# Kernel optimization log

Measured on AMD Instinct MI355X. Metric: run time of the kernel, lower is better.

## Reference

```python
import jax, jax.numpy as jnp
import numpy as np

V = 32000      # vocab
TMAX = 1024    # BLOCK_SIZE
D = 768        # N_EMBD
H = 12         # N_HEAD
L = 12         # N_LAYER
HS = D // H    # head_size
FF = 4 * D
B, T = 4, 1024


def setup_inputs() -> dict:
    key = jax.random.key(0)
    ks = iter(jax.random.split(key, 40))
    n = lambda shape: 0.02 * jax.random.normal(next(ks), shape, dtype=jnp.float32)
    return dict(
        idx=jax.random.randint(next(ks), (B, T), 0, V),
        targets=jax.random.randint(next(ks), (B, T), 0, V),
        tok_emb=n((V, D)),
        pos_emb=n((TMAX, D)),
        Wq=n((L, H, D, HS)), Wk=n((L, H, D, HS)), Wv=n((L, H, D, HS)),
        Wo=n((L, D, D)), bo=jnp.zeros((L, D)),
        W1=n((L, D, FF)), b1=jnp.zeros((L, FF)),
        W2=n((L, FF, D)), b2=jnp.zeros((L, D)),
        ln1_g=jnp.ones((L, D)), ln1_b=jnp.zeros((L, D)),
        ln2_g=jnp.ones((L, D)), ln2_b=jnp.zeros((L, D)),
        lnf_g=jnp.ones((D,)), lnf_b=jnp.zeros((D,)),
        Wlm=n((D, V)), blm=jnp.zeros((V,)),
    )


def _ln(x, g, b, eps=1e-5):
    m = x.mean(-1, keepdims=True)
    v = x.var(-1, keepdims=True)
    return (x - m) * jax.lax.rsqrt(v + eps) * g + b


def reference(idx, targets, tok_emb, pos_emb, Wq, Wk, Wv, Wo, bo,
              W1, b1, W2, b2, ln1_g, ln1_b, ln2_g, ln2_b, lnf_g, lnf_b,
              Wlm, blm):
    Bsz, Tt = idx.shape
    x = tok_emb[idx] + pos_emb[:Tt]                      # [B,T,D]
    causal = jnp.tril(jnp.ones((Tt, Tt), dtype=bool))     # [T,T]

    def layer(x, p):
        wq, wk, wv, wo, bob, w1, b1b, w2, b2b, g1, be1, g2, be2 = p
        h = _ln(x, g1, be1)
        q = jnp.einsum('btd,hdk->bhtk', h, wq)
        k = jnp.einsum('btd,hdk->bhtk', h, wk)
        v = jnp.einsum('btd,hdk->bhtk', h, wv)
        wei = jnp.einsum('bhtk,bhsk->bhts', q, k) * (HS ** -0.5)
        wei = jnp.where(causal, wei, -jnp.inf)
        wei = jax.nn.softmax(wei, axis=-1)                # dropout=0 in eval
        att = jnp.einsum('bhts,bhsk->bhtk', wei, v)
        att = att.transpose(0, 2, 1, 3).reshape(Bsz, Tt, H * HS)  # concat heads
        x = x + att @ wo + bob
        h2 = _ln(x, g2, be2)
        x = x + jax.nn.relu(h2 @ w1 + b1b) @ w2 + b2b
        return x, None

    x, _ = jax.lax.scan(layer, x,
                        (Wq, Wk, Wv, Wo, bo, W1, b1, W2, b2,
                         ln1_g, ln1_b, ln2_g, ln2_b))
    x = _ln(x, lnf_g, lnf_b)
    logits = x @ Wlm + blm                                # [B,T,V]
    lf = logits.reshape(Bsz * Tt, V)
    tf = targets.reshape(-1)
    logp = jax.nn.log_softmax(lf, axis=-1)
    loss = -jnp.take_along_axis(logp, tf[:, None], axis=1).mean()
    return lf, loss
```

## Files before the change

### kernel.cpp

```cpp
#include <hip/hip_runtime.h>

constexpr int C_B   = 4;
constexpr int C_T   = 1024;
constexpr int C_D   = 768;
constexpr int C_H   = 12;
constexpr int C_HS  = 64;
constexpr int C_FF  = 3072;
constexpr int C_V   = 32000;
constexpr int C_L   = 12;
constexpr int ROWS  = C_B * C_T;
constexpr int QKVN  = 3 * C_D;
constexpr int NCB   = C_V / 256;

typedef __bf16 bf16;
typedef __attribute__((ext_vector_type(8))) __bf16 bf16x8;
typedef __attribute__((ext_vector_type(4))) float  f32x4;
typedef __attribute__((ext_vector_type(4))) short  s16x4;

static __device__ __forceinline__ void gload16(const void* g, void* l) {
  __builtin_amdgcn_global_load_lds((const __attribute__((address_space(1))) void*)g,
                                   (__attribute__((address_space(3))) void*)l,
                                   16, 0, 0);
}

__global__ __launch_bounds__(256) void embed_kernel(const int* __restrict__ idx,
    const float* __restrict__ tok, const float* __restrict__ pos, float* __restrict__ x) {
  int gid = blockIdx.x * 256 + threadIdx.x;
  int row = gid / C_D, d = gid - row * C_D;
  int t = row & (C_T - 1);
  x[gid] = tok[(long)idx[row] * C_D + d] + pos[(long)t * C_D + d];
}

__global__ __launch_bounds__(256) void ln_kernel(const float* __restrict__ x,
    const float* __restrict__ g, const float* __restrict__ bb, long goff,
    bf16* __restrict__ out) {
  int row = blockIdx.x, tid = threadIdx.x;
  const float* xr = x + (long)row * C_D;
  float v0 = xr[tid], v1 = xr[tid + 256], v2 = xr[tid + 512];
  float s = v0 + v1 + v2;
  float s2 = v0 * v0 + v1 * v1 + v2 * v2;
#pragma unroll
  for (int off = 32; off > 0; off >>= 1) {
    s  += __shfl_down(s, off);
    s2 += __shfl_down(s2, off);
  }
  __shared__ float sm[4], sq[4];
  if ((tid & 63) == 0) { sm[tid >> 6] = s; sq[tid >> 6] = s2; }
  __syncthreads();
  s  = sm[0] + sm[1] + sm[2] + sm[3];
  s2 = sq[0] + sq[1] + sq[2] + sq[3];
  float mean = s * (1.f / C_D);
  float var  = s2 * (1.f / C_D) - mean * mean;
  float rstd = rsqrtf(var + 1e-5f);
  bf16* orow = out + (long)row * C_D;
  orow[tid]       = (bf16)((v0 - mean) * rstd * g[goff + tid]       + bb[goff + tid]);
  orow[tid + 256] = (bf16)((v1 - mean) * rstd * g[goff + tid + 256] + bb[goff + tid + 256]);
  orow[tid + 512] = (bf16)((v2 - mean) * rstd * g[goff + tid + 512] + bb[goff + tid + 512]);
}

__global__ __launch_bounds__(256) void transpose_kernel(const float* __restrict__ src,
    bf16* __restrict__ dst, int K, int N, long soff0, int ntn) {
  __shared__ bf16 tile[32][33];
  const float* s = src + soff0;
  int tn = blockIdx.x % ntn, tk = blockIdx.x / ntn;
  int c = threadIdx.x & 31, r = threadIdx.x >> 5;
#pragma unroll
  for (int it = 0; it < 4; ++it)
    tile[r + 8 * it][c] = (bf16)s[(long)(tk * 32 + r + 8 * it) * N + tn * 32 + c];
  __syncthreads();
#pragma unroll
  for (int it = 0; it < 4; ++it)
    dst[(long)(tn * 32 + r + 8 * it) * K + tk * 32 + c] = tile[c][r + 8 * it];
}

__global__ __launch_bounds__(256) void transpose_layer_kernel(
    const float* __restrict__ Wq, const float* __restrict__ Wk,
    const float* __restrict__ Wv, const float* __restrict__ Wo,
    const float* __restrict__ W1, const float* __restrict__ W2,
    bf16* __restrict__ wqkvt, bf16* __restrict__ wot,
    bf16* __restrict__ w1t, bf16* __restrict__ w2t, int l) {
  int bid = blockIdx.x;
  const float* src; bf16* dst; int K, N, ntn, t;
  if (bid < 1728) {
    int which = bid / 576, r = bid % 576, head = r / 48;
    t = r % 48;
    const float* W = which == 0 ? Wq : which == 1 ? Wk : Wv;
    src = W + (long)l * C_H * C_D * C_HS + (long)head * C_D * C_HS;
    dst = wqkvt + (long)which * C_D * C_D + (long)head * C_HS * C_D;
    K = C_D; N = C_HS; ntn = 2;
  } else if (bid < 2304) {
    t = bid - 1728; src = Wo + (long)l * C_D * C_D; dst = wot;
    K = C_D; N = C_D; ntn = 24;
  } else if (bid < 4608) {
    t = bid - 2304; src = W1 + (long)l * C_D * C_FF; dst = w1t;
    K = C_D; N = C_FF; ntn = 96;
  } else {
    t = bid - 4608; src = W2 + (long)l * C_FF * C_D; dst = w2t;
    K = C_FF; N = C_D; ntn = 24;
  }
  __shared__ bf16 tile[32][33];
  int tn = t % ntn, tk = t / ntn;
  int c = threadIdx.x & 31, r = threadIdx.x >> 5;
#pragma unroll
  for (int it = 0; it < 4; ++it)
    tile[r + 8 * it][c] = (bf16)src[(long)(tk * 32 + r + 8 * it) * N + tn * 32 + c];
  __syncthreads();
#pragma unroll
  for (int it = 0; it < 4; ++it)
    dst[(long)(tn * 32 + r + 8 * it) * K + tk * 32 + c] = tile[c][r + 8 * it];
}

__global__ __launch_bounds__(512) void gemm256(const bf16* __restrict__ A,
    const bf16* __restrict__ Bt, const float* __restrict__ bias, long boff,
    float* __restrict__ outp, float* __restrict__ lossp, int N, int K) {
  __shared__ __attribute__((aligned(16))) char smem[131072];
  int tid = threadIdx.x;
  int l = tid & 63, w = tid >> 6;
  int wm = w >> 2, wn = w & 3;
  int lg = l >> 4, lr = l & 15;

  int nwg = gridDim.x;
  int fid = blockIdx.x;
  int swz = (fid & 7) * (nwg >> 3) + (fid >> 3);
  long row0 = (long)(swz & 15) * 256;
  long col0 = (long)(swz >> 4) * 256;
  int cbi = (int)(col0 >> 8);

  int Y0 = tid * 16, Y1 = 8192 + tid * 16;
  auto dec = [](int Y, int& R, int& C) {
    int s = Y >> 10, y = Y & 1023;
    int r15 = y >> 6, z = y & 63;
    int q = (z ^ ((r15 & 8) << 2)) >> 4;
    R = (s >> 1) * 16 + r15;
    C = (s & 1) * 32 + q * 8;
  };
  int R0, C0, R1, C1;
  dec(Y0, R0, C0);  dec(Y1, R1, C1);
  const bf16* Ab = A  + row0 * K;
  const bf16* Bb = Bt + col0 * K;

  auto stage = [&](int d, int kt) {
    char* bb = smem + d * 65536;
    long kc = (long)kt * 64;
    gload16(Ab + (long)R0 * K + kc + C0, bb + Y0);
    gload16(Ab + (long)R1 * K + kc + C1, bb + Y1);
    gload16(Ab + (long)(128 + R0) * K + kc + C0, bb + 16384 + Y0);
    gload16(Ab + (long)(128 + R1) * K + kc + C1, bb + 16384 + Y1);
    gload16(Bb + (long)R0 * K + kc + C0, bb + 32768 + Y0);
    gload16(Bb + (long)R1 * K + kc + C1, bb + 32768 + Y1);
    gload16(Bb + (long)(128 + R0) * K + kc + C0, bb + 49152 + Y0);
    gload16(Bb + (long)(128 + R1) * K + kc + C1, bb + 49152 + Y1);
  };

  f32x4 acc[8][4];
  const f32x4 fz = {0.f, 0.f, 0.f, 0.f};
#pragma unroll
  for (int mf = 0; mf < 8; ++mf)
#pragma unroll
    for (int nf = 0; nf < 4; ++nf) acc[mf][nf] = fz;

  int aoff = lr * 64 + ((lg * 16) ^ ((lr & 8) << 2));
  int nk = K >> 6;
  stage(0, 0);
  int d = 0;
  for (int kt = 0; kt < nk; ++kt) {
    __syncthreads();
    if (kt + 1 < nk) stage(d ^ 1, kt + 1);
    const char* bB = smem + d * 65536 + 32768 + (wn >> 1) * 16384;
    bf16x8 bfrag[4][2];
#pragma unroll
    for (int nf = 0; nf < 4; ++nf)
#pragma unroll
      for (int k = 0; k < 2; ++k)
        bfrag[nf][k] = *(const bf16x8*)(bB + ((((wn & 1) * 4 + nf) * 2 + k) << 10) + aoff);
#pragma unroll
    for (int p = 0; p < 4; ++p) {
      bf16x8 af[2][2];
#pragma unroll
      for (int mi = 0; mi < 2; ++mi)
#pragma unroll
        for (int k = 0; k < 2; ++k) {
          int f = p * 2 + mi;
          const char* aB = smem + d * 65536 + (f >> 2) * 16384;
          af[mi][k] = *(const bf16x8*)(aB + (((wm * 4 + (f & 3)) * 2 + k) << 10) + aoff);
        }
      __builtin_amdgcn_s_setprio(1);
#pragma unroll
      for (int mi = 0; mi < 2; ++mi)
#pragma unroll
        for (int nf = 0; nf < 4; ++nf)
#pragma unroll
          for (int k = 0; k < 2; ++k)
            acc[p * 2 + mi][nf] = __builtin_amdgcn_mfma_f32_16x16x32_bf16(
                af[mi][k], bfrag[nf][k], acc[p * 2 + mi][nf], 0, 0, 0);
      __builtin_amdgcn_s_setprio(0);
    }
    d ^= 1;
  }
  __syncthreads();

#pragma unroll
  for (int h = 0; h < 2; ++h) {
    if (h) __syncthreads();
    float* lf = (float*)smem;
#pragma unroll
    for (int fq = 0; fq < 4; ++fq) {
      int f = h * 4 + fq;
      int rl = wm * 64 + fq * 16 + lg * 4;
#pragma unroll
      for (int nf = 0; nf < 4; ++nf) {
        int col = wn * 64 + nf * 16 + lr;
        float bv = bias ? bias[boff + col0 + col] : 0.f;
#pragma unroll
        for (int r = 0; r < 4; ++r)
          lf[(rl + r) * 256 + col] = acc[f][nf][r] + bv;
      }
    }
    __syncthreads();
#pragma unroll
    for (int it = 0; it < 16; ++it) {
      int byte = it * 8192 + tid * 16;
      int rl = byte >> 10, cb = byte & 1023;
      *(f32x4*)(outp + (row0 + h * 128 + rl) * N + col0 + (cb >> 2)) =
          *(const f32x4*)(smem + byte);
    }
    if (lossp) {
      const float* lfc = (const float*)smem;
      int row = tid >> 2, chunk = tid & 3;
      float M = -1e30f, S = 0.f;
#pragma unroll
      for (int j = 0; j < 16; ++j) {
        int jj = (j + row) & 15;
        f32x4 v = *(const f32x4*)(lfc + row * 256 + chunk * 64 + jj * 4);
#pragma unroll
        for (int q = 0; q < 4; ++q) {
          float xv = v[q];
          if (xv > M) { S *= __expf(M - xv); M = xv; }
          S += __expf(xv - M);
        }
      }
#pragma unroll
      for (int off = 1; off < 4; off <<= 1) {
        float Mo = __shfl_xor(M, off), So = __shfl_xor(S, off);
        float Mn = fmaxf(M, Mo);
        S = S * __expf(M - Mn) + So * __expf(Mo - Mn);
        M = Mn;
      }
      if (chunk == 0) {
        long pi = ((row0 + h * 128 + row) * NCB + cbi) * 2;
        lossp[pi] = M;  lossp[pi + 1] = S;
      }
    }
  }
}

template <int MODE>
__global__ __launch_bounds__(256) void gemm_bt(const bf16* __restrict__ A,
    const bf16* __restrict__ Bt, const float* __restrict__ bias, long boff,
    void* __restrict__ outp, float* __restrict__ resid, int N, int K) {
  __shared__ __attribute__((aligned(16))) char smem[32768];
  int tid = threadIdx.x;
  int l = tid & 63;
  int w = tid >> 6, wr = w >> 1, wc = w & 1;
  int lg = l >> 4, lr = l & 15;

  int nwg = gridDim.x;
  int fid = blockIdx.x;
  int swz = (fid & 7) * (nwg >> 3) + (fid >> 3);
  long row0 = (long)(swz & 31) * 128;
  long col0 = (long)(swz >> 5) * 128;

  const bf16* ga = A  + (row0 + (tid >> 2)) * K + (tid & 3) * 8;
  const bf16* gb = Bt + (col0 + (tid >> 2)) * K + (tid & 3) * 8;

  f32x4 acc[4][4];
  const f32x4 fz = {0.f, 0.f, 0.f, 0.f};
#pragma unroll
  for (int m = 0; m < 4; ++m)
#pragma unroll
    for (int n = 0; n < 4; ++n) acc[m][n] = fz;

  int nk = K >> 5;
  {
    bf16* la = (bf16*)smem + tid * 8;
    bf16* lb = (bf16*)(smem + 8192) + tid * 8;
    gload16(ga, la);  gload16(ga + (long)64 * K, la + 2048);
    gload16(gb, lb);  gload16(gb + (long)64 * K, lb + 2048);
    ga += 32; gb += 32;
  }
  int cur = 0;
  for (int t = 0; t < nk; ++t) {
    __syncthreads();
    if (t + 1 < nk) {
      char* bufb = smem + (cur ^ 1) * 16384;
      bf16* la = (bf16*)bufb + tid * 8;
      bf16* lb = (bf16*)(bufb + 8192) + tid * 8;
      gload16(ga, la);  gload16(ga + (long)64 * K, la + 2048);
      gload16(gb, lb);  gload16(gb + (long)64 * K, lb + 2048);
      ga += 32; gb += 32;
    }
    const bf16* cA = (const bf16*)(smem + cur * 16384);
    const bf16* cB = (const bf16*)(smem + cur * 16384 + 8192);
    bf16x8 af[4], bfr[4];
#pragma unroll
    for (int m = 0; m < 4; ++m)
      af[m] = *(const bf16x8*)(cA + (wr * 64 + m * 16 + lr) * 32 + lg * 8);
#pragma unroll
    for (int n = 0; n < 4; ++n)
      bfr[n] = *(const bf16x8*)(cB + (wc * 64 + n * 16 + lr) * 32 + lg * 8);
#pragma unroll
    for (int m = 0; m < 4; ++m)
#pragma unroll
      for (int n = 0; n < 4; ++n)
        acc[m][n] = __builtin_amdgcn_mfma_f32_16x16x32_bf16(af[m], bfr[n], acc[m][n], 0, 0, 0);
    cur ^= 1;
  }
  __syncthreads();

  if (MODE == 0 || MODE == 1) {
    bf16* lc = (bf16*)smem;
#pragma unroll
    for (int n = 0; n < 4; ++n) {
      int gcl = wc * 64 + n * 16 + lr;
      float bv = bias ? bias[boff + col0 + gcl] : 0.f;
#pragma unroll
      for (int m = 0; m < 4; ++m) {
        int rb = wr * 64 + m * 16 + lg * 4;
#pragma unroll
        for (int r = 0; r < 4; ++r) {
          float v = acc[m][n][r] + bv;
          if (MODE == 1) v = fmaxf(v, 0.f);
          lc[(rb + r) * 128 + gcl] = (bf16)v;
        }
      }
    }
    __syncthreads();
#pragma unroll
    for (int it = 0; it < 8; ++it) {
      int byte = it * 4096 + tid * 16;
      int rl = byte >> 8;
      int cb = byte & 255;
      *(bf16x8*)((bf16*)outp + (row0 + rl) * N + col0 + (cb >> 1)) =
          *(const bf16x8*)(smem + byte);
    }
  } else {
#pragma unroll
    for (int pair = 0; pair < 2; ++pair) {
      float* lcf = (float*)smem;
#pragma unroll
      for (int n = 0; n < 4; ++n) {
        int gcl = wc * 64 + n * 16 + lr;
        float bv = bias ? bias[boff + col0 + gcl] : 0.f;
#pragma unroll
        for (int mi = 0; mi < 2; ++mi) {
          int m = pair * 2 + mi;
          int rl = wr * 32 + mi * 16 + lg * 4;
#pragma unroll
          for (int r = 0; r < 4; ++r)
            lcf[(rl + r) * 128 + gcl] = acc[m][n][r] + bv;
        }
      }
      __syncthreads();
#pragma unroll
      for (int it = 0; it < 8; ++it) {
        int byte = it * 4096 + tid * 16;
        int rl = byte >> 9;
        int cb = byte & 511;
        long gr = row0 + (rl >> 5) * 64 + pair * 32 + ((rl >> 4) & 1) * 16 + (rl & 15);
        f32x4 v = *(const f32x4*)(smem + byte);
        f32x4 g = *(const f32x4*)(resid + gr * N + col0 + (cb >> 2));
        v += g;
        *(f32x4*)(resid + gr * N + col0 + (cb >> 2)) = v;
      }
      __syncthreads();
    }
  }
}

#define TRRD(D, OFF) asm volatile("ds_read_b64_tr_b16 %0, %1 offset:" OFF \
                                  : "=v"(D) : "v"(trp))
__global__ __launch_bounds__(64) void attn_kernel(const bf16* __restrict__ qkv,
                                                  bf16* __restrict__ attout) {
  int fid = blockIdx.x;
  int swzb = (fid & 7) * 384 + (fid >> 3);
  int qt = swzb & 63;
  int bh = swzb >> 6;
  int b = bh / C_H, h = bh % C_H;
  int l = threadIdx.x;
  int lg = l >> 4, lr = l & 15;
  const bf16* base = qkv + (long)b * C_T * QKVN;

  const bf16* qp = base + (long)(qt * 16 + lr) * QKVN + h * C_HS;
  bf16x8 qf0 = *(const bf16x8*)(qp + lg * 8);
  bf16x8 qf1 = *(const bf16x8*)(qp + 32 + lg * 8);

  const f32x4 fz = {0.f, 0.f, 0.f, 0.f};
  f32x4 o[4] = {fz, fz, fz, fz};
  float m_run[4], l_run[4];
#pragma unroll
  for (int r = 0; r < 4; ++r) { m_run[r] = -1e30f; l_run[r] = 0.f; }

  __shared__ __attribute__((aligned(16))) bf16 p_lds[16][40];
  __shared__ __attribute__((aligned(16))) bf16 vt_sub[2048];

  unsigned trp = (unsigned)(unsigned long)
      ((const __attribute__((address_space(3))) char*)vt_sub + l * 8);

  int nkt = (qt * 16 + 15) / 32 + 1;
  for (int kt = 0; kt < nkt; ++kt) {
    int key0 = kt * 32;
    f32x4 sacc[2];
#pragma unroll
    for (int ss = 0; ss < 2; ++ss) {
      const bf16* kp = base + (long)(key0 + ss * 16 + lr) * QKVN + C_D + h * C_HS;
      bf16x8 kf0 = *(const bf16x8*)(kp + lg * 8);
      bf16x8 kf1 = *(const bf16x8*)(kp + 32 + lg * 8);
      f32x4 a = fz;
      a = __builtin_amdgcn_mfma_f32_16x16x32_bf16(qf0, kf0, a, 0, 0, 0);
      a = __builtin_amdgcn_mfma_f32_16x16x32_bf16(qf1, kf1, a, 0, 0, 0);
      sacc[ss] = a;
    }
#pragma unroll
    for (int r = 0; r < 4; ++r) {
      int qrow = qt * 16 + lg * 4 + r;
      bool u0 = (key0 + lr) <= qrow;
      bool u1 = (key0 + 16 + lr) <= qrow;
      float s0 = u0 ? sacc[0][r] * 0.125f : -1e30f;
      float s1 = u1 ? sacc[1][r] * 0.125f : -1e30f;
      float mr = fmaxf(s0, s1);
      mr = fmaxf(mr, __shfl_xor(mr, 1));
      mr = fmaxf(mr, __shfl_xor(mr, 2));
      mr = fmaxf(mr, __shfl_xor(mr, 4));
      mr = fmaxf(mr, __shfl_xor(mr, 8));
      float mnew = fmaxf(m_run[r], mr);
      float scale = __expf(m_run[r] - mnew);
      float p0 = u0 ? __expf(s0 - mnew) : 0.f;
      float p1 = u1 ? __expf(s1 - mnew) : 0.f;
      float rs = p0 + p1;
      rs += __shfl_xor(rs, 1);
      rs += __shfl_xor(rs, 2);
      rs += __shfl_xor(rs, 4);
      rs += __shfl_xor(rs, 8);
      l_run[r] = l_run[r] * scale + rs;
      m_run[r] = mnew;
      o[0][r] *= scale; o[1][r] *= scale; o[2][r] *= scale; o[3][r] *= scale;
      p_lds[lg * 4 + r][lr]      = (bf16)p0;
      p_lds[lg * 4 + r][16 + lr] = (bf16)p1;
    }
#pragma unroll
    for (int it = 0; it < 4; ++it) {
      int kl = it * 8 + (l >> 3);
      int d0 = (l & 7) * 8;
      bf16x8 vv = *(const bf16x8*)(base + (long)(key0 + kl) * QKVN + 2 * C_D + h * C_HS + d0);
      int ba = ((d0 >> 4) << 10) + (((kl >> 2) & 1) << 9) + ((kl >> 3) << 7)
             + ((kl & 3) << 5) + ((d0 & 15) << 1);
      *(bf16x8*)((char*)vt_sub + ba) = vv;
    }
    __syncthreads();
    s16x4 t0a, t0b, t1a, t1b, t2a, t2b, t3a, t3b;
    TRRD(t0a, "0");    TRRD(t0b, "512");
    TRRD(t1a, "1024"); TRRD(t1b, "1536");
    TRRD(t2a, "2048"); TRRD(t2b, "2560");
    TRRD(t3a, "3072"); TRRD(t3b, "3584");
    bf16x8 pf = *(const bf16x8*)(&p_lds[lr][lg * 8]);
    asm volatile("s_waitcnt lgkmcnt(0)" ::: "memory");
    __builtin_amdgcn_sched_barrier(0);
    union uu { short s[8]; bf16x8 v; };
    auto mk = [](s16x4 a, s16x4 bq) {
      uu u;
      u.s[0] = a[0]; u.s[1] = a[1]; u.s[2] = a[2]; u.s[3] = a[3];
      u.s[4] = bq[0]; u.s[5] = bq[1]; u.s[6] = bq[2]; u.s[7] = bq[3];
      return u.v;
    };
    o[0] = __builtin_amdgcn_mfma_f32_16x16x32_bf16(pf, mk(t0a, t0b), o[0], 0, 0, 0);
    o[1] = __builtin_amdgcn_mfma_f32_16x16x32_bf16(pf, mk(t1a, t1b), o[1], 0, 0, 0);
    o[2] = __builtin_amdgcn_mfma_f32_16x16x32_bf16(pf, mk(t2a, t2b), o[2], 0, 0, 0);
    o[3] = __builtin_amdgcn_mfma_f32_16x16x32_bf16(pf, mk(t3a, t3b), o[3], 0, 0, 0);
    __syncthreads();
  }
#pragma unroll
  for (int c = 0; c < 4; ++c)
#pragma unroll
    for (int r = 0; r < 4; ++r) {
      int qrow = qt * 16 + lg * 4 + r;
      attout[((long)b * C_T + qrow) * C_D + h * C_HS + c * 16 + lr] =
          (bf16)(o[c][r] / l_run[r]);
    }
}

__global__ __launch_bounds__(128) void loss_partial_kernel(const float* __restrict__ lossp,
    const float* __restrict__ logits, const int* __restrict__ targets,
    float* __restrict__ rowloss) {
  int row = blockIdx.x * 128 + threadIdx.x;
  const float* pp = lossp + (long)row * NCB * 2;
  float M = -1e30f, S = 0.f;
  for (int i = 0; i < NCB; ++i) {
    float pm = pp[i * 2], ps = pp[i * 2 + 1];
    float Mn = fmaxf(M, pm);
    S = S * __expf(M - Mn) + ps * __expf(pm - Mn);
    M = Mn;
  }
  float lt = logits[(long)row * C_V + targets[row]];
  rowloss[row] = -(lt - M - logf(S));
}

__global__ __launch_bounds__(256) void loss_final(const float* __restrict__ rowloss,
                                                  float* __restrict__ out) {
  int tid = threadIdx.x;
  float s = 0.f;
  for (int i = tid; i < ROWS; i += 256) s += rowloss[i];
#pragma unroll
  for (int off = 32; off > 0; off >>= 1) s += __shfl_down(s, off);
  __shared__ float sm[4];
  if ((tid & 63) == 0) sm[tid >> 6] = s;
  __syncthreads();
  if (tid == 0) out[0] = (sm[0] + sm[1] + sm[2] + sm[3]) * (1.f / ROWS);
}

extern "C" void kernel_launch(void* const* d_in, const int* in_sizes, int n_in,
                              void* d_out, int out_size, void* d_ws, size_t ws_size,
                              hipStream_t stream) {
  (void)in_sizes; (void)n_in; (void)out_size; (void)ws_size;
  const int*   idx     = (const int*)  d_in[0];
  const int*   targets = (const int*)  d_in[1];
  const float* tok     = (const float*)d_in[2];
  const float* pos     = (const float*)d_in[3];
  const float* Wq      = (const float*)d_in[4];
  const float* Wk      = (const float*)d_in[5];
  const float* Wv      = (const float*)d_in[6];
  const float* Wo      = (const float*)d_in[7];
  const float* bo      = (const float*)d_in[8];
  const float* W1      = (const float*)d_in[9];
  const float* b1      = (const float*)d_in[10];
  const float* W2      = (const float*)d_in[11];
  const float* b2      = (const float*)d_in[12];
  const float* ln1g    = (const float*)d_in[13];
  const float* ln1b    = (const float*)d_in[14];
  const float* ln2g    = (const float*)d_in[15];
  const float* ln2b    = (const float*)d_in[16];
  const float* lnfg    = (const float*)d_in[17];
  const float* lnfb    = (const float*)d_in[18];
  const float* Wlm     = (const float*)d_in[19];
  const float* blm     = (const float*)d_in[20];

  char* p = (char*)d_ws;
  auto alloc = [&](size_t bytes) {
    char* r = p; p += (bytes + 255) & ~(size_t)255; return r;
  };
  float* x       = (float*)alloc((size_t)ROWS * C_D * 4);
  bf16*  h       = (bf16*) alloc((size_t)ROWS * C_D * 2);
  bf16*  qkv     = (bf16*) alloc((size_t)ROWS * QKVN * 2);
  bf16*  attout  = (bf16*) alloc((size_t)ROWS * C_D * 2);
  bf16*  ffbuf   = (bf16*) alloc((size_t)ROWS * C_FF * 2);
  bf16*  wqkvt   = (bf16*) alloc((size_t)QKVN * C_D * 2);
  bf16*  wot     = (bf16*) alloc((size_t)C_D * C_D * 2);
  bf16*  w1t     = (bf16*) alloc((size_t)C_FF * C_D * 2);
  bf16*  w2t     = (bf16*) alloc((size_t)C_D * C_FF * 2);
  float* rowloss = (float*)alloc((size_t)ROWS * 4);
  float* lossp   = (float*)alloc((size_t)ROWS * NCB * 2 * 4);
  bf16*  wlmt    = qkv;

  float* logits = (float*)d_out;

  embed_kernel<<<ROWS * C_D / 256, 256, 0, stream>>>(idx, tok, pos, x);

  for (int l = 0; l < C_L; ++l) {
    transpose_layer_kernel<<<6912, 256, 0, stream>>>(
        Wq, Wk, Wv, Wo, W1, W2, wqkvt, wot, w1t, w2t, l);

    ln_kernel<<<ROWS, 256, 0, stream>>>(x, ln1g, ln1b, (long)l * C_D, h);
    gemm_bt<0><<<(QKVN / 128) * 32, 256, 0, stream>>>(
        h, wqkvt, nullptr, 0, qkv, nullptr, QKVN, C_D);
    attn_kernel<<<C_B * C_H * (C_T / 16), 64, 0, stream>>>(qkv, attout);
    gemm_bt<2><<<(C_D / 128) * 32, 256, 0, stream>>>(
        attout, wot, bo, (long)l * C_D, nullptr, x, C_D, C_D);
    ln_kernel<<<ROWS, 256, 0, stream>>>(x, ln2g, ln2b, (long)l * C_D, h);
    gemm_bt<1><<<(C_FF / 128) * 32, 256, 0, stream>>>(
        h, w1t, b1, (long)l * C_FF, ffbuf, nullptr, C_FF, C_D);
    gemm_bt<2><<<(C_D / 128) * 32, 256, 0, stream>>>(
        ffbuf, w2t, b2, (long)l * C_D, nullptr, x, C_D, C_FF);
  }

  transpose_kernel<<<(C_V / 32) * (C_D / 32), 256, 0, stream>>>(
      Wlm, wlmt, C_D, C_V, 0, C_V / 32);

  ln_kernel<<<ROWS, 256, 0, stream>>>(x, lnfg, lnfb, 0, h);
  gemm256<<<16 * (C_V / 256), 512, 0, stream>>>(
      h, wlmt, blm, 0, logits, lossp, C_V, C_D);
  loss_partial_kernel<<<ROWS / 128, 128, 0, stream>>>(lossp, logits, targets, rowloss);
  loss_final<<<1, 256, 0, stream>>>(rowloss, logits + (long)ROWS * C_V);
}
```

Before: 2.981 ms.

## Add 128x64 residual GEMM kernel and split-barrier LM-head pipeline

Adds a new gemm_bt64 kernel with 128x64 tiles for the two N=768 residual-add GEMMs (attention output and FFN down projection), doubling the workgroup count from 192 to 384 so more CUs are used. Its epilogue writes the full fp32 tile in one pass instead of two. The LM-head GEMM loop now issues the next stage's loads, waits with an explicit vmcnt, and uses a raw s_barrier pair in place of __syncthreads, so the wait on outstanding global-to-LDS loads is controlled by hand. The smaller tiles lower reuse per workgroup, and the hand-written waitcnt depends on exactly how many loads stage issues.

```diff
diff --git a/kernel.cpp b/kernel.cpp
--- a/kernel.cpp
+++ b/kernel.cpp
@@ -164,8 +164,17 @@
   stage(0, 0);
   int d = 0;
   for (int kt = 0; kt < nk; ++kt) {
-    __syncthreads();
-    if (kt + 1 < nk) stage(d ^ 1, kt + 1);
+    __builtin_amdgcn_s_barrier();
+    asm volatile("" ::: "memory");
+    if (kt + 1 < nk) {
+      stage(d ^ 1, kt + 1);
+      asm volatile("s_waitcnt vmcnt(8)" ::: "memory");
+    } else {
+      asm volatile("s_waitcnt vmcnt(0)" ::: "memory");
+    }
+    __builtin_amdgcn_s_barrier();
+    asm volatile("" ::: "memory");
+
     const char* bB = smem + d * 65536 + 32768 + (wn >> 1) * 16384;
     bf16x8 bfrag[4][2];
 #pragma unroll
@@ -257,7 +266,7 @@
 template <int MODE>
 __global__ __launch_bounds__(256) void gemm_bt(const bf16* __restrict__ A,
     const bf16* __restrict__ Bt, const float* __restrict__ bias, long boff,
-    void* __restrict__ outp, float* __restrict__ resid, int N, int K) {
+    void* __restrict__ outp, int N, int K) {
   __shared__ __attribute__((aligned(16))) char smem[32768];
   int tid = threadIdx.x;
   int l = tid & 63;
@@ -317,63 +326,119 @@
   }
   __syncthreads();
 
-  if (MODE == 0 || MODE == 1) {
-    bf16* lc = (bf16*)smem;
-#pragma unroll
-    for (int n = 0; n < 4; ++n) {
-      int gcl = wc * 64 + n * 16 + lr;
-      float bv = bias ? bias[boff + col0 + gcl] : 0.f;
-#pragma unroll
-      for (int m = 0; m < 4; ++m) {
-        int rb = wr * 64 + m * 16 + lg * 4;
-#pragma unroll
-        for (int r = 0; r < 4; ++r) {
-          float v = acc[m][n][r] + bv;
-          if (MODE == 1) v = fmaxf(v, 0.f);
-          lc[(rb + r) * 128 + gcl] = (bf16)v;
-        }
+  bf16* lc = (bf16*)smem;
+#pragma unroll
+  for (int n = 0; n < 4; ++n) {
+    int gcl = wc * 64 + n * 16 + lr;
+    float bv = bias ? bias[boff + col0 + gcl] : 0.f;
+#pragma unroll
+    for (int m = 0; m < 4; ++m) {
+      int rb = wr * 64 + m * 16 + lg * 4;
+#pragma unroll
+      for (int r = 0; r < 4; ++r) {
+        float v = acc[m][n][r] + bv;
+        if (MODE == 1) v = fmaxf(v, 0.f);
+        lc[(rb + r) * 128 + gcl] = (bf16)v;
       }
     }
+  }
+  __syncthreads();
+#pragma unroll
+  for (int it = 0; it < 8; ++it) {
+    int byte = it * 4096 + tid * 16;
+    int rl = byte >> 8;
+    int cb = byte & 255;
+    *(bf16x8*)((bf16*)outp + (row0 + rl) * N + col0 + (cb >> 1)) =
+        *(const bf16x8*)(smem + byte);
+  }
+}
+
+__global__ __launch_bounds__(256) void gemm_bt64(const bf16* __restrict__ A,
+    const bf16* __restrict__ Bt, const float* __restrict__ bias, long boff,
+    float* __restrict__ resid, int N, int K) {
+  __shared__ __attribute__((aligned(16))) char smem[32768];
+  int tid = threadIdx.x;
+  int l = tid & 63;
+  int w = tid >> 6, wr = w >> 1, wc = w & 1;
+  int lg = l >> 4, lr = l & 15;
+
+  int nwg = gridDim.x;
+  int fid = blockIdx.x;
+  int swz = (fid & 7) * (nwg >> 3) + (fid >> 3);
+  long row0 = (long)(swz & 31) * 128;
+  long col0 = (long)(swz >> 5) * 64;
+
+  const bf16* ga = A  + (row0 + (tid >> 2)) * K + (tid & 3) * 8;
+  const bf16* gb = Bt + (col0 + (tid >> 2)) * K + (tid & 3) * 8;
+
+  f32x4 acc[4][2];
+  const f32x4 fz = {0.f, 0.f, 0.f, 0.f};
+#pragma unroll
+  for (int m = 0; m < 4; ++m)
+#pragma unroll
+    for (int n = 0; n < 2; ++n) acc[m][n] = fz;
+
+  int nk = K >> 5;
+  {
+    bf16* la = (bf16*)smem + tid * 8;
+    bf16* lb = (bf16*)(smem + 8192) + tid * 8;
+    gload16(ga, la);  gload16(ga + (long)64 * K, la + 2048);
+    if (tid < 256) gload16(gb, lb);
+    ga += 32; gb += 32;
+  }
+  int cur = 0;
+  for (int t = 0; t < nk; ++t) {
     __syncthreads();
-#pragma unroll
-    for (int it = 0; it < 8; ++it) {
-      int byte = it * 4096 + tid * 16;
-      int rl = byte >> 8;
-      int cb = byte & 255;
-      *(bf16x8*)((bf16*)outp + (row0 + rl) * N + col0 + (cb >> 1)) =
-          *(const bf16x8*)(smem + byte);
-    }
-  } else {
-#pragma unroll
-    for (int pair = 0; pair < 2; ++pair) {
-      float* lcf = (float*)smem;
-#pragma unroll
-      for (int n = 0; n < 4; ++n) {
-        int gcl = wc * 64 + n * 16 + lr;
-        float bv = bias ? bias[boff + col0 + gcl] : 0.f;
-#pragma unroll
-        for (int mi = 0; mi < 2; ++mi) {
-          int m = pair * 2 + mi;
-          int rl = wr * 32 + mi * 16 + lg * 4;
-#pragma unroll
-          for (int r = 0; r < 4; ++r)
-            lcf[(rl + r) * 128 + gcl] = acc[m][n][r] + bv;
-        }
-      }
-      __syncthreads();
-#pragma unroll
-      for (int it = 0; it < 8; ++it) {
-        int byte = it * 4096 + tid * 16;
-        int rl = byte >> 9;
-        int cb = byte & 511;
-        long gr = row0 + (rl >> 5) * 64 + pair * 32 + ((rl >> 4) & 1) * 16 + (rl & 15);
-        f32x4 v = *(const f32x4*)(smem + byte);
-        f32x4 g = *(const f32x4*)(resid + gr * N + col0 + (cb >> 2));
-        v += g;
-        *(f32x4*)(resid + gr * N + col0 + (cb >> 2)) = v;
-      }
-      __syncthreads();
-    }
+    if (t + 1 < nk) {
+      char* bufb = smem + (cur ^ 1) * 12288;
+      bf16* la = (bf16*)bufb + tid * 8;
+      bf16* lb = (bf16*)(bufb + 8192) + tid * 8;
+      gload16(ga, la);  gload16(ga + (long)64 * K, la + 2048);
+      gload16(gb, lb);
+      ga += 32; gb += 32;
+    }
+    const bf16* cA = (const bf16*)(smem + cur * 12288);
+    const bf16* cB = (const bf16*)(smem + cur * 12288 + 8192);
+    bf16x8 af[4], bfr[2];
+#pragma unroll
+    for (int m = 0; m < 4; ++m)
+      af[m] = *(const bf16x8*)(cA + (wr * 64 + m * 16 + lr) * 32 + lg * 8);
+#pragma unroll
+    for (int n = 0; n < 2; ++n)
+      bfr[n] = *(const bf16x8*)(cB + (wc * 32 + n * 16 + lr) * 32 + lg * 8);
+#pragma unroll
+    for (int m = 0; m < 4; ++m)
+#pragma unroll
+      for (int n = 0; n < 2; ++n)
+        acc[m][n] = __builtin_amdgcn_mfma_f32_16x16x32_bf16(af[m], bfr[n], acc[m][n], 0, 0, 0);
+    cur ^= 1;
+  }
+  __syncthreads();
+
+  float* lcf = (float*)smem;
+#pragma unroll
+  for (int n = 0; n < 2; ++n) {
+    int col = wc * 32 + n * 16 + lr;
+    float bv = bias ? bias[boff + col0 + col] : 0.f;
+#pragma unroll
+    for (int m = 0; m < 4; ++m) {
+      int rl = wr * 64 + m * 16 + lg * 4;
+#pragma unroll
+      for (int r = 0; r < 4; ++r)
+        lcf[(rl + r) * 64 + col] = acc[m][n][r] + bv;
+    }
+  }
+  __syncthreads();
+#pragma unroll
+  for (int it = 0; it < 8; ++it) {
+    int byte = it * 4096 + tid * 16;
+    int rl = byte >> 8;
+    int cb = byte & 255;
+    long gr = row0 + rl;
+    f32x4 v = *(const f32x4*)(smem + byte);
+    f32x4 g = *(const f32x4*)(resid + gr * N + col0 + (cb >> 2));
+    v += g;
+    *(f32x4*)(resid + gr * N + col0 + (cb >> 2)) = v;
   }
 }
 
@@ -570,15 +635,15 @@
 
     ln_kernel<<<ROWS, 256, 0, stream>>>(x, ln1g, ln1b, (long)l * C_D, h);
     gemm_bt<0><<<(QKVN / 128) * 32, 256, 0, stream>>>(
-        h, wqkvt, nullptr, 0, qkv, nullptr, QKVN, C_D);
+        h, wqkvt, nullptr, 0, qkv, QKVN, C_D);
     attn_kernel<<<C_B * C_H * (C_T / 16), 64, 0, stream>>>(qkv, attout);
-    gemm_bt<2><<<(C_D / 128) * 32, 256, 0, stream>>>(
-        attout, wot, bo, (long)l * C_D, nullptr, x, C_D, C_D);
+    gemm_bt64<<<(C_D / 64) * 32, 256, 0, stream>>>(
+        attout, wot, bo, (long)l * C_D, x, C_D, C_D);
     ln_kernel<<<ROWS, 256, 0, stream>>>(x, ln2g, ln2b, (long)l * C_D, h);
     gemm_bt<1><<<(C_FF / 128) * 32, 256, 0, stream>>>(
-        h, w1t, b1, (long)l * C_FF, ffbuf, nullptr, C_FF, C_D);
-    gemm_bt<2><<<(C_D / 128) * 32, 256, 0, stream>>>(
-        ffbuf, w2t, b2, (long)l * C_D, nullptr, x, C_D, C_FF);
+        h, w1t, b1, (long)l * C_FF, ffbuf, C_FF, C_D);
+    gemm_bt64<<<(C_D / 64) * 32, 256, 0, stream>>>(
+        ffbuf, w2t, b2, (long)l * C_D, x, C_D, C_FF);
   }
 
   transpose_kernel<<<(C_V / 32) * (C_D / 32), 256, 0, stream>>>(
```

Result: faster. 2.805 ms (-5.9%).
